# Kernel optimization log

Measured on AMD Instinct MI355X. Metric: run time of the kernel, lower is better.

The kernel has to match this reference:

```python
import jax, jax.numpy as jnp
import numpy as np

N_NODES = 128
F = 64            # hidden channels (64x0e + 64x1o)
N_RBF = 8
H_R = 64          # radial MLP hidden
L = 2             # num_interactions
R_MAX = 5.0
AVG_NEIGH = 127.0
G_DIM = 16
N_SPECIES = 5

# static fully-connected edge list (no self edges): E = n*(n-1)
_idx = np.arange(N_NODES)
_s, _r = np.meshgrid(_idx, _idx, indexing='ij')
_mask = _s != _r
SENDERS = jnp.asarray(_s[_mask])    # [E]
RECEIVERS = jnp.asarray(_r[_mask])  # [E]


def setup_inputs() -> dict:
    key = jax.random.key(0)
    ks = jax.random.split(key, 12)
    inp = {
        'positions': jax.random.normal(ks[0], (32, N_NODES, 3), jnp.float32),
        'node_features': jax.random.randint(ks[1], (32, N_NODES), 0, N_SPECIES),
        'global_features': jax.random.normal(ks[2], (32, G_DIM), jnp.float32),
        # learned parameters
        'embed': jax.random.normal(ks[3], (N_SPECIES, F), jnp.float32) * 0.1,
        'glob_w': jax.random.normal(ks[4], (G_DIM, F), jnp.float32) * 0.1,
        'rbf_w1': jax.random.normal(ks[5], (L, N_RBF, H_R), jnp.float32) * 0.3,
        'rbf_b1': jnp.zeros((L, H_R), jnp.float32),
        'rbf_w2': jax.random.normal(ks[6], (L, H_R, 3 * F), jnp.float32) * 0.1,
        'ws': jax.random.normal(ks[7], (L, F, F), jnp.float32) * 0.1,
        'wv': jax.random.normal(ks[8], (L, F, F), jnp.float32) * 0.1,
        'wout': jax.random.normal(ks[9], (F,), jnp.float32) * 0.1,
        'final_scaling': jnp.ones((), jnp.float32),
    }
    return inp


def _rbf(d):
    # gaussian radial basis on [0, r_max]
    centers = jnp.linspace(0.0, R_MAX, N_RBF)
    width = R_MAX / N_RBF
    return jnp.exp(-((d[:, None] - centers) ** 2) / (2.0 * width * width))  # [E, N_RBF]


def _single(pos, species, glob, embed, glob_w, rbf_w1, rbf_b1, rbf_w2, ws, wv, wout, final_scaling):
    # graph construction + edge vectors
    edge_vec = pos[RECEIVERS] - pos[SENDERS]                 # [E,3]
    d = jnp.sqrt(jnp.sum(edge_vec ** 2, axis=-1) + 1e-12)   # [E]
    unit = edge_vec / d[:, None]                             # [E,3]
    phi = _rbf(d)                                            # [E,N_RBF]

    # node embedding (species one-hot lookup) conditioned on global features
    s = embed[species] + glob @ glob_w                       # [n,F] scalars
    v = jnp.zeros((N_NODES, F, 3), pos.dtype)                # [n,F,3] vectors

    for l in range(L):
        rw = jax.nn.silu(phi @ rbf_w1[l] + rbf_b1[l]) @ rbf_w2[l]  # [E,3F]
        r1, r2, r3 = jnp.split(rw, 3, axis=-1)               # each [E,F]
        ms = r1 * s[SENDERS]                                 # [E,F]
        mv = r2[..., None] * v[SENDERS] + (r3 * s[SENDERS])[..., None] * unit[:, None, :]  # [E,F,3]
        agg_s = jax.ops.segment_sum(ms, RECEIVERS, num_segments=N_NODES) / AVG_NEIGH
        agg_v = jax.ops.segment_sum(mv, RECEIVERS, num_segments=N_NODES) / AVG_NEIGH
        s = s + agg_s @ ws[l]
        v = v + jnp.einsum('nfd,fg->ngd', agg_v, wv[l])

    out = jnp.einsum('nfd,f->nd', v, wout)                   # equivariant readout [n,3]
    return (out - pos) * final_scaling


def reference(positions, node_features, global_features, embed, glob_w, rbf_w1,
              rbf_b1, rbf_w2, ws, wv, wout, final_scaling):
    fn = lambda p, sp, g: _single(p, sp, g, embed, glob_w, rbf_w1, rbf_b1,
                                  rbf_w2, ws, wv, wout, final_scaling)
    return jax.vmap(fn)(positions, node_features, global_features)
```

## Files before the change

kernel.cpp:

```cpp
#include <hip/hip_runtime.h>
#include <hip/hip_bf16.h>


#define NN 128
#define BB 32
#define FF 64

using f32x4  = __attribute__((ext_vector_type(4))) float;
using short8 = __attribute__((ext_vector_type(8))) short;
using half4  = __attribute__((ext_vector_type(4))) _Float16;

__device__ __forceinline__ unsigned short f2bf(float x) {
    unsigned int u = __float_as_uint(x);
    u += 0x7fff + ((u >> 16) & 1);
    return (unsigned short)(u >> 16);
}
__device__ __forceinline__ unsigned int f2bf_fast32(float x) {
    return (__float_as_uint(x) + 0x8000u) >> 16;
}

__global__ __launch_bounds__(256) void setup_kernel(
    const float* __restrict__ w2,
    const float* __restrict__ ws,
    const float* __restrict__ wv,
    const float* __restrict__ rbf_w1,
    const float* __restrict__ rbf_b1,
    const int* __restrict__ species, const float* __restrict__ glob,
    const float* __restrict__ embed, const float* __restrict__ glob_w,
    short* __restrict__ w2frag,
    float* __restrict__ wT4,
    _Float16* __restrict__ w1A,
    float* __restrict__ s)
{
    const int blk = blockIdx.x;
    if (blk < 192) {
        const int tid = blk * 256 + threadIdx.x;
        const int NFRAG = 24576;
        if (tid < NFRAG) {
            const int e  = tid & 7;
            const int l  = (tid >> 3) & 63;
            const int ks = (tid >> 9) & 1;
            const int q  = tid >> 10;
            const int nt = q % 3;
            const int wv_ = (q / 3) & 3;
            const int layer = q / 12;
            const int col = nt * 64 + wv_ * 16 + (l & 15);
            const int hb  = ks * 32 + (l >> 4) * 8 + e;
            const float val = w2[layer * 64 * 192 + hb * 192 + col] * (1.0f / 127.0f);
            w2frag[tid] = (short)f2bf(val);
        }
        const int tid2 = tid - NFRAG;
        if (tid2 >= 0 && tid2 < 16384) {
            const int c   = tid2 & 3;
            const int g   = (tid2 >> 2) & 63;
            const int ff4 = (tid2 >> 8) & 15;
            const int m   = (tid2 >> 12) & 1;
            const int layer = tid2 >> 13;
            const float* src = (m == 0 ? ws : wv) + layer * 4096;
            wT4[tid2] = src[(ff4 * 4 + c) * 64 + g];
        }
        const int tid3 = tid - NFRAG - 16384;
        if (tid3 >= 0 && tid3 < 2048) {
            const int e  = tid3 & 3;
            const int l  = (tid3 >> 2) & 63;
            const int wv_ = (tid3 >> 8) & 3;
            const int layer = tid3 >> 10;
            const int k = (l >> 4) * 4 + e;
            const int h = wv_ * 16 + (l & 15);
            float val = 0.0f;
            if (k < 8)       val = rbf_w1[layer * 512 + k * 64 + h];
            else if (k == 8) val = rbf_b1[layer * 64 + h];
            w1A[tid3] = (_Float16)val;
        }
    } else {
        const int node = (blk - 192) * 4 + (threadIdx.x >> 6);
        const int b = node >> 7;
        const int f = threadIdx.x & 63;
        const int sp = species[node];
        float acc = embed[sp * FF + f];
#pragma unroll
        for (int k = 0; k < 16; ++k)
            acc = fmaf(glob[b * 16 + k], glob_w[k * FF + f], acc);
        s[node * FF + f] = acc;
    }
}

template<int LAYER>
__global__ __launch_bounds__(256, 2) void msg_kernel(
    const float* __restrict__ pos,
    const float* __restrict__ s_in,
    const float* __restrict__ v_in,
    const half4* __restrict__ w1Abuf,
    const short* __restrict__ w2frag,
    const float* __restrict__ wT4,
    const float* __restrict__ wout,
    const float* __restrict__ scale,
    float* __restrict__ s_out,
    float* __restrict__ v_out,
    float* __restrict__ out)
{
    __shared__ unsigned short hid_lds[NN * 64];
    __shared__ float4 unit_lds[NN];
    __shared__ __align__(16) char phi_pool[NN * 32];
    float4 (*agg4)[16] = (float4(*)[16])phi_pool;

    const int blk = blockIdx.x;
    const int xcd = blk & 7;
    const int idx = blk >> 3;
    const int b = xcd * 4 + (idx >> 7);
    const int i = idx & 127;

    const int t = threadIdx.x;
    const int w = t >> 6;
    const int l = t & 63;
    const int node = b * NN + i;
    const float* pb = pos + b * NN * 3;

    short8 bfrag[3][2];
    {
        const short8* wf = (const short8*)w2frag;
#pragma unroll
        for (int nt = 0; nt < 3; ++nt) {
            if (LAYER == 0 && nt == 1) continue;
#pragma unroll
            for (int ks = 0; ks < 2; ++ks)
                bfrag[nt][ks] = wf[((w * 3 + nt) * 2 + ks) * 64 + l];
        }
    }

    {
        const int j = t & 127;
        const int half = t >> 7;
        const float dx = pb[i * 3 + 0] - pb[j * 3 + 0];
        const float dy = pb[i * 3 + 1] - pb[j * 3 + 1];
        const float dz = pb[i * 3 + 2] - pb[j * 3 + 2];
        const float d2 = fmaf(dx, dx, fmaf(dy, dy, fmaf(dz, dz, 1e-12f)));
        const float inv = __builtin_amdgcn_rsqf(d2);
        const float dd = d2 * inv;
        if (half == 0)
            unit_lds[j] = make_float4(dx * inv, dy * inv, dz * inv, 0.0f);
        const _Float16 zf = (_Float16)0.f;
        half4 ph;
#pragma unroll
        for (int r = 0; r < 4; ++r) {
            const float td = dd - (float)(half * 4 + r) * (5.0f / 7.0f);
            ph[r] = (_Float16)__expf(td * td * -1.28f);
        }
        if (j == i) ph = (half4){zf, zf, zf, zf};
        char* rowp = phi_pool + j * 32;
        const int swz = ((j >> 2) & 3) << 3;
        *(half4*)(rowp + ((half * 8) ^ swz)) = ph;
        if (half == 0) {
            half4 bias = {(j == i) ? zf : (_Float16)1.0f, zf, zf, zf};
            *(half4*)(rowp + (16 ^ swz)) = bias;
        } else {
            *(half4*)(rowp + (24 ^ swz)) = (half4){zf, zf, zf, zf};
        }
    }
    __syncthreads();

    {
        const half4 w1a = w1Abuf[w * 64 + l];
        const int jcol = l & 15;
        const int chunk = (l >> 4) * 8;
        const int hbyte = w * 32 + (l >> 4) * 8;
#pragma unroll
        for (int mt = 0; mt < 8; ++mt) {
            const int j = mt * 16 + jcol;
            const half4 bphi = *(const half4*)(
                phi_pool + j * 32 + (chunk ^ (((j >> 2) & 3) << 3)));
            f32x4 pre = __builtin_amdgcn_mfma_f32_16x16x16f16(
                w1a, bphi, (f32x4){0.f, 0.f, 0.f, 0.f}, 0, 0, 0);
            unsigned int pk[2];
#pragma unroll
            for (int p = 0; p < 2; ++p) {
                float sv[2];
#pragma unroll
                for (int q = 0; q < 2; ++q) {
                    const float z = pre[p * 2 + q];
                    const float ex = __expf(-z);
                    sv[q] = z * __builtin_amdgcn_rcpf(1.0f + ex);
                }
                pk[p] = f2bf_fast32(sv[0]) | (f2bf_fast32(sv[1]) << 16);
            }
            const int byte = j * 128 + (hbyte ^ ((j & 7) << 4));
            *(uint2*)((char*)hid_lds + byte) = make_uint2(pk[0], pk[1]);
        }
    }
    __syncthreads();

    const int f    = w * 16 + (l & 15);
    const int jsub = (l >> 4) * 4;
    const float* sb = s_in + b * NN * FF;
    const float4* vb4 = (LAYER > 0) ? ((const float4*)v_in) + b * NN * FF : nullptr;

    float accs = 0.f, av0 = 0.f, av1 = 0.f, av2 = 0.f;

    float sP[4]; float4 vP[4];
#pragma unroll
    for (int reg = 0; reg < 4; ++reg) {
        const int j = jsub + reg;
        sP[reg] = sb[j * FF + f];
        if (LAYER > 0) vP[reg] = vb4[j * FF + f];
    }

#pragma unroll
    for (int mt = 0; mt < 8; ++mt) {
        const int jA = mt * 16 + (l & 15);
        const int base = jA * 128;
        const int sw = (jA & 7) << 4;
        const short8 a0 = *(const short8*)((const char*)hid_lds + base + (((l >> 4) * 16 +  0) ^ sw));
        const short8 a1 = *(const short8*)((const char*)hid_lds + base + (((l >> 4) * 16 + 64) ^ sw));

        f32x4 c0 = (f32x4){0.f, 0.f, 0.f, 0.f};
        f32x4 c1 = (f32x4){0.f, 0.f, 0.f, 0.f};
        f32x4 c2 = (f32x4){0.f, 0.f, 0.f, 0.f};
        c0 = __builtin_amdgcn_mfma_f32_16x16x32_bf16(a0, bfrag[0][0], c0, 0, 0, 0);
        c0 = __builtin_amdgcn_mfma_f32_16x16x32_bf16(a1, bfrag[0][1], c0, 0, 0, 0);
        if (LAYER > 0) {
            c1 = __builtin_amdgcn_mfma_f32_16x16x32_bf16(a0, bfrag[1][0], c1, 0, 0, 0);
            c1 = __builtin_amdgcn_mfma_f32_16x16x32_bf16(a1, bfrag[1][1], c1, 0, 0, 0);
        }
        c2 = __builtin_amdgcn_mfma_f32_16x16x32_bf16(a0, bfrag[2][0], c2, 0, 0, 0);
        c2 = __builtin_amdgcn_mfma_f32_16x16x32_bf16(a1, bfrag[2][1], c2, 0, 0, 0);

        float sN[4]; float4 vN[4];
        if (mt < 7) {
#pragma unroll
            for (int reg = 0; reg < 4; ++reg) {
                const int j = (mt + 1) * 16 + jsub + reg;
                sN[reg] = sb[j * FF + f];
                if (LAYER > 0) vN[reg] = vb4[j * FF + f];
            }
        }

#pragma unroll
        for (int reg = 0; reg < 4; ++reg) {
            const int j  = mt * 16 + jsub + reg;
            const float r1 = c0[reg];
            const float r2 = c1[reg];
            const float r3 = c2[reg];
            const float sj = sP[reg];
            const float r3s = r3 * sj;
            const float4 u = unit_lds[j];
            accs = fmaf(r1, sj, accs);
            av0 = fmaf(r3s, u.x, av0);
            av1 = fmaf(r3s, u.y, av1);
            av2 = fmaf(r3s, u.z, av2);
            if (LAYER > 0) {
                av0 = fmaf(r2, vP[reg].x, av0);
                av1 = fmaf(r2, vP[reg].y, av1);
                av2 = fmaf(r2, vP[reg].z, av2);
            }
        }
#pragma unroll
        for (int reg = 0; reg < 4; ++reg) {
            sP[reg] = sN[reg];
            if (LAYER > 0) vP[reg] = vN[reg];
        }
    }

    accs += __shfl_xor(accs, 16, 64); accs += __shfl_xor(accs, 32, 64);
    av0  += __shfl_xor(av0, 16, 64);  av0  += __shfl_xor(av0, 32, 64);
    av1  += __shfl_xor(av1, 16, 64);  av1  += __shfl_xor(av1, 32, 64);
    av2  += __shfl_xor(av2, 16, 64);  av2  += __shfl_xor(av2, 32, 64);
    if (l < 16) {
        ((float*)agg4)[0 * 64 + f] = accs;
        ((float*)agg4)[1 * 64 + f] = av0;
        ((float*)agg4)[2 * 64 + f] = av1;
        ((float*)agg4)[3 * 64 + f] = av2;
    }
    __syncthreads();

    const int g = l;
    const float4* wv4 = (const float4*)wT4;
    if (LAYER == 0) {
        const int m = (w == 0) ? 0 : 1;
        const int row = (w == 0) ? 0 : w;
        float a = (w == 0) ? s_in[node * FF + g] : 0.0f;
#pragma unroll
        for (int k = 0; k < 16; ++k) {
            const float4 w4 = wv4[(m * 16 + k) * 64 + g];
            const float4 a4 = agg4[row][k];
            a = fmaf(a4.x, w4.x, a); a = fmaf(a4.y, w4.y, a);
            a = fmaf(a4.z, w4.z, a); a = fmaf(a4.w, w4.w, a);
        }
        if (w == 0) s_out[node * FF + g] = a;
        else        v_out[(node * FF + g) * 4 + (w - 1)] = a;
    } else {
        if (w > 0) {
            const int d = w - 1;
            float a = v_in[(node * FF + g) * 4 + d];
#pragma unroll
            for (int k = 0; k < 16; ++k) {
                const float4 w4 = wv4[(16 + k) * 64 + g];
                const float4 a4 = agg4[w][k];
                a = fmaf(a4.x, w4.x, a); a = fmaf(a4.y, w4.y, a);
                a = fmaf(a4.z, w4.z, a); a = fmaf(a4.w, w4.w, a);
            }
            float p = a * wout[g];
#pragma unroll
            for (int off = 1; off < 64; off <<= 1)
                p += __shfl_xor(p, off, 64);
            if (l == 0)
                out[node * 3 + d] = (p - pos[node * 3 + d]) * scale[0];
        }
    }
}

extern "C" void kernel_launch(void* const* d_in, const int* in_sizes, int n_in,
                              void* d_out, int out_size, void* d_ws, size_t ws_size,
                              hipStream_t stream) {
    const float* pos     = (const float*)d_in[0];
    const int*   species = (const int*)  d_in[1];
    const float* glob    = (const float*)d_in[2];
    const float* embed   = (const float*)d_in[3];
    const float* glob_w  = (const float*)d_in[4];
    const float* rbf_w1  = (const float*)d_in[5];
    const float* rbf_b1  = (const float*)d_in[6];
    const float* rbf_w2  = (const float*)d_in[7];
    const float* ws      = (const float*)d_in[8];
    const float* wv      = (const float*)d_in[9];
    const float* wout    = (const float*)d_in[10];
    const float* scale   = (const float*)d_in[11];

    float* wsf = (float*)d_ws;
    float* s0     = wsf;
    float* s1     = wsf + 262144;
    float* v1     = wsf + 524288;
    short* w2frag = (short*)(wsf + 1572864);
    float* wT4    = wsf + 1585152;
    _Float16* w1A = (_Float16*)(wsf + 1601536);
    float* outp = (float*)d_out;

    setup_kernel<<<dim3(192 + BB * NN / 4), 256, 0, stream>>>(
        rbf_w2, ws, wv, rbf_w1, rbf_b1, species, glob, embed, glob_w,
        w2frag, wT4, w1A, s0);

    msg_kernel<0><<<dim3(NN * BB), 256, 0, stream>>>(
        pos, s0, nullptr,
        (const half4*)w1A, w2frag, wT4, wout, scale,
        s1, v1, nullptr);

    msg_kernel<1><<<dim3(NN * BB), 256, 0, stream>>>(
        pos, s1, v1,
        (const half4*)(w1A + 1024), w2frag + 12288, wT4 + 8192, wout, scale,
        nullptr, nullptr, outp);
}
```

Before: 78.95 us.

## Process two receiver nodes per 512-thread block in message kernel

Each message block now handles two receiver nodes using 512 threads (8 waves), with LDS buffers doubled and indexed per node. Grid size is halved. The aim is to amortize per-block fixed costs such as weight-fragment loads and syncs, and to improve occupancy via launch bounds of 512 threads with 4 blocks. The trade-offs are higher LDS use per block and a tighter register budget under the new launch bounds, which may cause spills.

After: 83.56 us. 5.8% more time.

```diff
diff --git a/kernel.cpp b/kernel.cpp
--- a/kernel.cpp
+++ b/kernel.cpp
@@ -86,7 +86,7 @@
 }
 
 template<int LAYER>
-__global__ __launch_bounds__(256, 2) void msg_kernel(
+__global__ __launch_bounds__(512, 4) void msg_kernel(
     const float* __restrict__ pos,
     const float* __restrict__ s_in,
     const float* __restrict__ v_in,
@@ -99,21 +99,23 @@
     float* __restrict__ v_out,
     float* __restrict__ out)
 {
-    __shared__ unsigned short hid_lds[NN * 64];
-    __shared__ float4 unit_lds[NN];
-    __shared__ __align__(16) char phi_pool[NN * 32];
-    float4 (*agg4)[16] = (float4(*)[16])phi_pool;
+    __shared__ unsigned short hid_lds[2 * NN * 64];
+    __shared__ float4 unit_lds[2 * NN];
+    __shared__ __align__(16) char phi_pool[2 * NN * 32];
+    float* aggf = (float*)phi_pool;
 
     const int blk = blockIdx.x;
     const int xcd = blk & 7;
     const int idx = blk >> 3;
-    const int b = xcd * 4 + (idx >> 7);
-    const int i = idx & 127;
+    const int b = xcd * 4 + (idx >> 6);
+    const int ipair = idx & 63;
 
     const int t = threadIdx.x;
     const int w = t >> 6;
     const int l = t & 63;
-    const int node = b * NN + i;
+    const int r = w >> 2;
+    const int ws = w & 3;
+    const int i = ipair * 2 + r;
     const float* pb = pos + b * NN * 3;
 
     short8 bfrag[3][2];
@@ -124,34 +126,36 @@
             if (LAYER == 0 && nt == 1) continue;
 #pragma unroll
             for (int ks = 0; ks < 2; ++ks)
-                bfrag[nt][ks] = wf[((w * 3 + nt) * 2 + ks) * 64 + l];
+                bfrag[nt][ks] = wf[((ws * 3 + nt) * 2 + ks) * 64 + l];
         }
     }
 
     {
         const int j = t & 127;
-        const int half = t >> 7;
-        const float dx = pb[i * 3 + 0] - pb[j * 3 + 0];
-        const float dy = pb[i * 3 + 1] - pb[j * 3 + 1];
-        const float dz = pb[i * 3 + 2] - pb[j * 3 + 2];
+        const int rr = (t >> 7) & 1;
+        const int half = t >> 8;
+        const int ie = ipair * 2 + rr;
+        const float dx = pb[ie * 3 + 0] - pb[j * 3 + 0];
+        const float dy = pb[ie * 3 + 1] - pb[j * 3 + 1];
+        const float dz = pb[ie * 3 + 2] - pb[j * 3 + 2];
         const float d2 = fmaf(dx, dx, fmaf(dy, dy, fmaf(dz, dz, 1e-12f)));
         const float inv = __builtin_amdgcn_rsqf(d2);
         const float dd = d2 * inv;
         if (half == 0)
-            unit_lds[j] = make_float4(dx * inv, dy * inv, dz * inv, 0.0f);
+            unit_lds[rr * NN + j] = make_float4(dx * inv, dy * inv, dz * inv, 0.0f);
         const _Float16 zf = (_Float16)0.f;
         half4 ph;
 #pragma unroll
-        for (int r = 0; r < 4; ++r) {
-            const float td = dd - (float)(half * 4 + r) * (5.0f / 7.0f);
-            ph[r] = (_Float16)__expf(td * td * -1.28f);
-        }
-        if (j == i) ph = (half4){zf, zf, zf, zf};
-        char* rowp = phi_pool + j * 32;
+        for (int rbf = 0; rbf < 4; ++rbf) {
+            const float td = dd - (float)(half * 4 + rbf) * (5.0f / 7.0f);
+            ph[rbf] = (_Float16)__expf(td * td * -1.28f);
+        }
+        if (j == ie) ph = (half4){zf, zf, zf, zf};
+        char* rowp = phi_pool + rr * 4096 + j * 32;
         const int swz = ((j >> 2) & 3) << 3;
         *(half4*)(rowp + ((half * 8) ^ swz)) = ph;
         if (half == 0) {
-            half4 bias = {(j == i) ? zf : (_Float16)1.0f, zf, zf, zf};
+            half4 bias = {(j == ie) ? zf : (_Float16)1.0f, zf, zf, zf};
             *(half4*)(rowp + (16 ^ swz)) = bias;
         } else {
             *(half4*)(rowp + (24 ^ swz)) = (half4){zf, zf, zf, zf};
@@ -160,15 +164,17 @@
     __syncthreads();
 
     {
-        const half4 w1a = w1Abuf[w * 64 + l];
+        const half4 w1a = w1Abuf[ws * 64 + l];
         const int jcol = l & 15;
         const int chunk = (l >> 4) * 8;
-        const int hbyte = w * 32 + (l >> 4) * 8;
+        const int hbyte = ws * 32 + (l >> 4) * 8;
+        const char* phir = phi_pool + r * 4096;
+        char* hidr = (char*)hid_lds + r * 16384;
 #pragma unroll
         for (int mt = 0; mt < 8; ++mt) {
             const int j = mt * 16 + jcol;
             const half4 bphi = *(const half4*)(
-                phi_pool + j * 32 + (chunk ^ (((j >> 2) & 3) << 3)));
+                phir + j * 32 + (chunk ^ (((j >> 2) & 3) << 3)));
             f32x4 pre = __builtin_amdgcn_mfma_f32_16x16x16f16(
                 w1a, bphi, (f32x4){0.f, 0.f, 0.f, 0.f}, 0, 0, 0);
             unsigned int pk[2];
@@ -184,15 +190,17 @@
                 pk[p] = f2bf_fast32(sv[0]) | (f2bf_fast32(sv[1]) << 16);
             }
             const int byte = j * 128 + (hbyte ^ ((j & 7) << 4));
-            *(uint2*)((char*)hid_lds + byte) = make_uint2(pk[0], pk[1]);
+            *(uint2*)(hidr + byte) = make_uint2(pk[0], pk[1]);
         }
     }
     __syncthreads();
 
-    const int f    = w * 16 + (l & 15);
+    const int f    = ws * 16 + (l & 15);
     const int jsub = (l >> 4) * 4;
     const float* sb = s_in + b * NN * FF;
     const float4* vb4 = (LAYER > 0) ? ((const float4*)v_in) + b * NN * FF : nullptr;
+    const char* hidr = (const char*)hid_lds + r * 16384;
+    const float4* unitr = unit_lds + r * NN;
 
     float accs = 0.f, av0 = 0.f, av1 = 0.f, av2 = 0.f;
 
@@ -209,8 +217,8 @@
         const int jA = mt * 16 + (l & 15);
         const int base = jA * 128;
         const int sw = (jA & 7) << 4;
-        const short8 a0 = *(const short8*)((const char*)hid_lds + base + (((l >> 4) * 16 +  0) ^ sw));
-        const short8 a1 = *(const short8*)((const char*)hid_lds + base + (((l >> 4) * 16 + 64) ^ sw));
+        const short8 a0 = *(const short8*)(hidr + base + (((l >> 4) * 16 +  0) ^ sw));
+        const short8 a1 = *(const short8*)(hidr + base + (((l >> 4) * 16 + 64) ^ sw));
 
         f32x4 c0 = (f32x4){0.f, 0.f, 0.f, 0.f};
         f32x4 c1 = (f32x4){0.f, 0.f, 0.f, 0.f};
@@ -242,7 +250,7 @@
             const float r3 = c2[reg];
             const float sj = sP[reg];
             const float r3s = r3 * sj;
-            const float4 u = unit_lds[j];
+            const float4 u = unitr[j];
             accs = fmaf(r1, sj, accs);
             av0 = fmaf(r3s, u.x, av0);
             av1 = fmaf(r3s, u.y, av1);
@@ -265,36 +273,38 @@
     av1  += __shfl_xor(av1, 16, 64);  av1  += __shfl_xor(av1, 32, 64);
     av2  += __shfl_xor(av2, 16, 64);  av2  += __shfl_xor(av2, 32, 64);
     if (l < 16) {
-        ((float*)agg4)[0 * 64 + f] = accs;
-        ((float*)agg4)[1 * 64 + f] = av0;
-        ((float*)agg4)[2 * 64 + f] = av1;
-        ((float*)agg4)[3 * 64 + f] = av2;
+        aggf[r * 256 + 0 * 64 + f] = accs;
+        aggf[r * 256 + 1 * 64 + f] = av0;
+        aggf[r * 256 + 2 * 64 + f] = av1;
+        aggf[r * 256 + 3 * 64 + f] = av2;
     }
     __syncthreads();
 
     const int g = l;
+    const int node = b * NN + i;
     const float4* wv4 = (const float4*)wT4;
+    const float4* agg4 = ((const float4*)phi_pool) + r * 64;
     if (LAYER == 0) {
-        const int m = (w == 0) ? 0 : 1;
-        const int row = (w == 0) ? 0 : w;
-        float a = (w == 0) ? s_in[node * FF + g] : 0.0f;
+        const int m = (ws == 0) ? 0 : 1;
+        const int row = ws;
+        float a = (ws == 0) ? s_in[node * FF + g] : 0.0f;
 #pragma unroll
         for (int k = 0; k < 16; ++k) {
             const float4 w4 = wv4[(m * 16 + k) * 64 + g];
-            const float4 a4 = agg4[row][k];
+            const float4 a4 = agg4[row * 16 + k];
             a = fmaf(a4.x, w4.x, a); a = fmaf(a4.y, w4.y, a);
             a = fmaf(a4.z, w4.z, a); a = fmaf(a4.w, w4.w, a);
         }
-        if (w == 0) s_out[node * FF + g] = a;
-        else        v_out[(node * FF + g) * 4 + (w - 1)] = a;
+        if (ws == 0) s_out[node * FF + g] = a;
+        else         v_out[(node * FF + g) * 4 + (ws - 1)] = a;
     } else {
-        if (w > 0) {
-            const int d = w - 1;
+        if (ws > 0) {
+            const int d = ws - 1;
             float a = v_in[(node * FF + g) * 4 + d];
 #pragma unroll
             for (int k = 0; k < 16; ++k) {
                 const float4 w4 = wv4[(16 + k) * 64 + g];
-                const float4 a4 = agg4[w][k];
+                const float4 a4 = agg4[ws * 16 + k];
                 a = fmaf(a4.x, w4.x, a); a = fmaf(a4.y, w4.y, a);
                 a = fmaf(a4.z, w4.z, a); a = fmaf(a4.w, w4.w, a);
             }
@@ -337,12 +347,12 @@
         rbf_w2, ws, wv, rbf_w1, rbf_b1, species, glob, embed, glob_w,
         w2frag, wT4, w1A, s0);
 
-    msg_kernel<0><<<dim3(NN * BB), 256, 0, stream>>>(
+    msg_kernel<0><<<dim3(NN * BB / 2), 512, 0, stream>>>(
         pos, s0, nullptr,
         (const half4*)w1A, w2frag, wT4, wout, scale,
         s1, v1, nullptr);
 
-    msg_kernel<1><<<dim3(NN * BB), 256, 0, stream>>>(
+    msg_kernel<1><<<dim3(NN * BB / 2), 512, 0, stream>>>(
         pos, s1, v1,
         (const half4*)(w1A + 1024), w2frag + 12288, wT4 + 8192, wout, scale,
         nullptr, nullptr, outp);
```

## Process four receiver nodes per block with double-buffered LDS pipeline

Applied to the files above, without the earlier changes.

Each block now handles four receiver nodes instead of one, cutting the grid by a factor of four and amortizing the per-block loads of weight fragments. LDS buffers for phi, the hidden activations and unit vectors are doubled so the edge setup and radial MLP of the next node can run alongside the message MFMAs and the tail of the current node. This removes per-block launch and setup overhead and separates dependent phases, at the cost of more LDS per block, which may lower occupancy, and fewer blocks to spread across CUs.

Result: slower. 109.1 us (+38.2%).

```diff
diff --git a/kernel.cpp b/kernel.cpp
--- a/kernel.cpp
+++ b/kernel.cpp
@@ -99,22 +99,26 @@
     float* __restrict__ v_out,
     float* __restrict__ out)
 {
-    __shared__ unsigned short hid_lds[NN * 64];
-    __shared__ float4 unit_lds[NN];
-    __shared__ __align__(16) char phi_pool[NN * 32];
-    float4 (*agg4)[16] = (float4(*)[16])phi_pool;
+    __shared__ unsigned short hid_lds[2][NN * 64];
+    __shared__ float4 unit_lds[2][NN];
+    __shared__ __align__(16) char phi_pool[2][NN * 32];
+    __shared__ float4 agg4[4][16];
 
     const int blk = blockIdx.x;
     const int xcd = blk & 7;
     const int idx = blk >> 3;
-    const int b = xcd * 4 + (idx >> 7);
-    const int i = idx & 127;
+    const int b = xcd * 4 + (idx >> 5);
+    const int i0 = (idx & 31) * 4;
 
     const int t = threadIdx.x;
     const int w = t >> 6;
     const int l = t & 63;
-    const int node = b * NN + i;
     const float* pb = pos + b * NN * 3;
+
+    const int f    = w * 16 + (l & 15);
+    const int jsub = (l >> 4) * 4;
+    const float* sb = s_in + b * NN * FF;
+    const float4* vb4 = (LAYER > 0) ? ((const float4*)v_in) + b * NN * FF : nullptr;
 
     short8 bfrag[3][2];
     {
@@ -127,48 +131,49 @@
                 bfrag[nt][ks] = wf[((w * 3 + nt) * 2 + ks) * 64 + l];
         }
     }
-
-    {
+    const half4 w1a = w1Abuf[w * 64 + l];
+
+    auto A1 = [&](int ie, int bf) {
         const int j = t & 127;
         const int half = t >> 7;
-        const float dx = pb[i * 3 + 0] - pb[j * 3 + 0];
-        const float dy = pb[i * 3 + 1] - pb[j * 3 + 1];
-        const float dz = pb[i * 3 + 2] - pb[j * 3 + 2];
+        const float dx = pb[ie * 3 + 0] - pb[j * 3 + 0];
+        const float dy = pb[ie * 3 + 1] - pb[j * 3 + 1];
+        const float dz = pb[ie * 3 + 2] - pb[j * 3 + 2];
         const float d2 = fmaf(dx, dx, fmaf(dy, dy, fmaf(dz, dz, 1e-12f)));
         const float inv = __builtin_amdgcn_rsqf(d2);
         const float dd = d2 * inv;
         if (half == 0)
-            unit_lds[j] = make_float4(dx * inv, dy * inv, dz * inv, 0.0f);
+            unit_lds[bf][j] = make_float4(dx * inv, dy * inv, dz * inv, 0.0f);
         const _Float16 zf = (_Float16)0.f;
         half4 ph;
 #pragma unroll
-        for (int r = 0; r < 4; ++r) {
-            const float td = dd - (float)(half * 4 + r) * (5.0f / 7.0f);
-            ph[r] = (_Float16)__expf(td * td * -1.28f);
-        }
-        if (j == i) ph = (half4){zf, zf, zf, zf};
-        char* rowp = phi_pool + j * 32;
+        for (int rr = 0; rr < 4; ++rr) {
+            const float td = dd - (float)(half * 4 + rr) * (5.0f / 7.0f);
+            ph[rr] = (_Float16)__expf(td * td * -1.28f);
+        }
+        if (j == ie) ph = (half4){zf, zf, zf, zf};
+        char* rowp = phi_pool[bf] + j * 32;
         const int swz = ((j >> 2) & 3) << 3;
         *(half4*)(rowp + ((half * 8) ^ swz)) = ph;
         if (half == 0) {
-            half4 bias = {(j == i) ? zf : (_Float16)1.0f, zf, zf, zf};
+            half4 bias = {(j == ie) ? zf : (_Float16)1.0f, zf, zf, zf};
             *(half4*)(rowp + (16 ^ swz)) = bias;
         } else {
             *(half4*)(rowp + (24 ^ swz)) = (half4){zf, zf, zf, zf};
         }
-    }
-    __syncthreads();
-
-    {
-        const half4 w1a = w1Abuf[w * 64 + l];
+    };
+
+    auto A2 = [&](int bf) {
         const int jcol = l & 15;
         const int chunk = (l >> 4) * 8;
         const int hbyte = w * 32 + (l >> 4) * 8;
+        const char* phir = phi_pool[bf];
+        char* hidr = (char*)hid_lds[bf];
 #pragma unroll
         for (int mt = 0; mt < 8; ++mt) {
             const int j = mt * 16 + jcol;
             const half4 bphi = *(const half4*)(
-                phi_pool + j * 32 + (chunk ^ (((j >> 2) & 3) << 3)));
+                phir + j * 32 + (chunk ^ (((j >> 2) & 3) << 3)));
             f32x4 pre = __builtin_amdgcn_mfma_f32_16x16x16f16(
                 w1a, bphi, (f32x4){0.f, 0.f, 0.f, 0.f}, 0, 0, 0);
             unsigned int pk[2];
@@ -184,127 +189,138 @@
                 pk[p] = f2bf_fast32(sv[0]) | (f2bf_fast32(sv[1]) << 16);
             }
             const int byte = j * 128 + (hbyte ^ ((j & 7) << 4));
-            *(uint2*)((char*)hid_lds + byte) = make_uint2(pk[0], pk[1]);
-        }
-    }
-    __syncthreads();
-
-    const int f    = w * 16 + (l & 15);
-    const int jsub = (l >> 4) * 4;
-    const float* sb = s_in + b * NN * FF;
-    const float4* vb4 = (LAYER > 0) ? ((const float4*)v_in) + b * NN * FF : nullptr;
-
-    float accs = 0.f, av0 = 0.f, av1 = 0.f, av2 = 0.f;
-
-    float sP[4]; float4 vP[4];
-#pragma unroll
-    for (int reg = 0; reg < 4; ++reg) {
-        const int j = jsub + reg;
-        sP[reg] = sb[j * FF + f];
-        if (LAYER > 0) vP[reg] = vb4[j * FF + f];
-    }
-
-#pragma unroll
-    for (int mt = 0; mt < 8; ++mt) {
-        const int jA = mt * 16 + (l & 15);
-        const int base = jA * 128;
-        const int sw = (jA & 7) << 4;
-        const short8 a0 = *(const short8*)((const char*)hid_lds + base + (((l >> 4) * 16 +  0) ^ sw));
-        const short8 a1 = *(const short8*)((const char*)hid_lds + base + (((l >> 4) * 16 + 64) ^ sw));
-
-        f32x4 c0 = (f32x4){0.f, 0.f, 0.f, 0.f};
-        f32x4 c1 = (f32x4){0.f, 0.f, 0.f, 0.f};
-        f32x4 c2 = (f32x4){0.f, 0.f, 0.f, 0.f};
-        c0 = __builtin_amdgcn_mfma_f32_16x16x32_bf16(a0, bfrag[0][0], c0, 0, 0, 0);
-        c0 = __builtin_amdgcn_mfma_f32_16x16x32_bf16(a1, bfrag[0][1], c0, 0, 0, 0);
-        if (LAYER > 0) {
-            c1 = __builtin_amdgcn_mfma_f32_16x16x32_bf16(a0, bfrag[1][0], c1, 0, 0, 0);
-            c1 = __builtin_amdgcn_mfma_f32_16x16x32_bf16(a1, bfrag[1][1], c1, 0, 0, 0);
-        }
-        c2 = __builtin_amdgcn_mfma_f32_16x16x32_bf16(a0, bfrag[2][0], c2, 0, 0, 0);
-        c2 = __builtin_amdgcn_mfma_f32_16x16x32_bf16(a1, bfrag[2][1], c2, 0, 0, 0);
-
-        float sN[4]; float4 vN[4];
-        if (mt < 7) {
+            *(uint2*)(hidr + byte) = make_uint2(pk[0], pk[1]);
+        }
+    };
+
+    auto BC = [&](int bf) {
+        const char* hidr = (const char*)hid_lds[bf];
+        const float4* unitr = unit_lds[bf];
+        float accs = 0.f, av0 = 0.f, av1 = 0.f, av2 = 0.f;
+        float sP[4]; float4 vP[4];
+#pragma unroll
+        for (int reg = 0; reg < 4; ++reg) {
+            const int j = jsub + reg;
+            sP[reg] = sb[j * FF + f];
+            if (LAYER > 0) vP[reg] = vb4[j * FF + f];
+        }
+#pragma unroll
+        for (int mt = 0; mt < 8; ++mt) {
+            const int jA = mt * 16 + (l & 15);
+            const int base = jA * 128;
+            const int sw = (jA & 7) << 4;
+            const short8 a0 = *(const short8*)(hidr + base + (((l >> 4) * 16 +  0) ^ sw));
+            const short8 a1 = *(const short8*)(hidr + base + (((l >> 4) * 16 + 64) ^ sw));
+
+            f32x4 c0 = (f32x4){0.f, 0.f, 0.f, 0.f};
+            f32x4 c1 = (f32x4){0.f, 0.f, 0.f, 0.f};
+            f32x4 c2 = (f32x4){0.f, 0.f, 0.f, 0.f};
+            c0 = __builtin_amdgcn_mfma_f32_16x16x32_bf16(a0, bfrag[0][0], c0, 0, 0, 0);
+            c0 = __builtin_amdgcn_mfma_f32_16x16x32_bf16(a1, bfrag[0][1], c0, 0, 0, 0);
+            if (LAYER > 0) {
+                c1 = __builtin_amdgcn_mfma_f32_16x16x32_bf16(a0, bfrag[1][0], c1, 0, 0, 0);
+                c1 = __builtin_amdgcn_mfma_f32_16x16x32_bf16(a1, bfrag[1][1], c1, 0, 0, 0);
+            }
+            c2 = __builtin_amdgcn_mfma_f32_16x16x32_bf16(a0, bfrag[2][0], c2, 0, 0, 0);
+            c2 = __builtin_amdgcn_mfma_f32_16x16x32_bf16(a1, bfrag[2][1], c2, 0, 0, 0);
+
+            float sN[4]; float4 vN[4];
+            if (mt < 7) {
+#pragma unroll
+                for (int reg = 0; reg < 4; ++reg) {
+                    const int j = (mt + 1) * 16 + jsub + reg;
+                    sN[reg] = sb[j * FF + f];
+                    if (LAYER > 0) vN[reg] = vb4[j * FF + f];
+                }
+            }
 #pragma unroll
             for (int reg = 0; reg < 4; ++reg) {
-                const int j = (mt + 1) * 16 + jsub + reg;
-                sN[reg] = sb[j * FF + f];
-                if (LAYER > 0) vN[reg] = vb4[j * FF + f];
-            }
-        }
-
-#pragma unroll
-        for (int reg = 0; reg < 4; ++reg) {
-            const int j  = mt * 16 + jsub + reg;
-            const float r1 = c0[reg];
-            const float r2 = c1[reg];
-            const float r3 = c2[reg];
-            const float sj = sP[reg];
-            const float r3s = r3 * sj;
-            const float4 u = unit_lds[j];
-            accs = fmaf(r1, sj, accs);
-            av0 = fmaf(r3s, u.x, av0);
-            av1 = fmaf(r3s, u.y, av1);
-            av2 = fmaf(r3s, u.z, av2);
-            if (LAYER > 0) {
-                av0 = fmaf(r2, vP[reg].x, av0);
-                av1 = fmaf(r2, vP[reg].y, av1);
-                av2 = fmaf(r2, vP[reg].z, av2);
-            }
-        }
-#pragma unroll
-        for (int reg = 0; reg < 4; ++reg) {
-            sP[reg] = sN[reg];
-            if (LAYER > 0) vP[reg] = vN[reg];
-        }
-    }
-
-    accs += __shfl_xor(accs, 16, 64); accs += __shfl_xor(accs, 32, 64);
-    av0  += __shfl_xor(av0, 16, 64);  av0  += __shfl_xor(av0, 32, 64);
-    av1  += __shfl_xor(av1, 16, 64);  av1  += __shfl_xor(av1, 32, 64);
-    av2  += __shfl_xor(av2, 16, 64);  av2  += __shfl_xor(av2, 32, 64);
-    if (l < 16) {
-        ((float*)agg4)[0 * 64 + f] = accs;
-        ((float*)agg4)[1 * 64 + f] = av0;
-        ((float*)agg4)[2 * 64 + f] = av1;
-        ((float*)agg4)[3 * 64 + f] = av2;
-    }
-    __syncthreads();
-
-    const int g = l;
-    const float4* wv4 = (const float4*)wT4;
-    if (LAYER == 0) {
-        const int m = (w == 0) ? 0 : 1;
-        const int row = (w == 0) ? 0 : w;
-        float a = (w == 0) ? s_in[node * FF + g] : 0.0f;
-#pragma unroll
-        for (int k = 0; k < 16; ++k) {
-            const float4 w4 = wv4[(m * 16 + k) * 64 + g];
-            const float4 a4 = agg4[row][k];
-            a = fmaf(a4.x, w4.x, a); a = fmaf(a4.y, w4.y, a);
-            a = fmaf(a4.z, w4.z, a); a = fmaf(a4.w, w4.w, a);
-        }
-        if (w == 0) s_out[node * FF + g] = a;
-        else        v_out[(node * FF + g) * 4 + (w - 1)] = a;
-    } else {
-        if (w > 0) {
-            const int d = w - 1;
-            float a = v_in[(node * FF + g) * 4 + d];
+                const int j  = mt * 16 + jsub + reg;
+                const float r1 = c0[reg];
+                const float r2 = c1[reg];
+                const float r3 = c2[reg];
+                const float sj = sP[reg];
+                const float r3s = r3 * sj;
+                const float4 u = unitr[j];
+                accs = fmaf(r1, sj, accs);
+                av0 = fmaf(r3s, u.x, av0);
+                av1 = fmaf(r3s, u.y, av1);
+                av2 = fmaf(r3s, u.z, av2);
+                if (LAYER > 0) {
+                    av0 = fmaf(r2, vP[reg].x, av0);
+                    av1 = fmaf(r2, vP[reg].y, av1);
+                    av2 = fmaf(r2, vP[reg].z, av2);
+                }
+            }
+#pragma unroll
+            for (int reg = 0; reg < 4; ++reg) {
+                sP[reg] = sN[reg];
+                if (LAYER > 0) vP[reg] = vN[reg];
+            }
+        }
+        accs += __shfl_xor(accs, 16, 64); accs += __shfl_xor(accs, 32, 64);
+        av0  += __shfl_xor(av0, 16, 64);  av0  += __shfl_xor(av0, 32, 64);
+        av1  += __shfl_xor(av1, 16, 64);  av1  += __shfl_xor(av1, 32, 64);
+        av2  += __shfl_xor(av2, 16, 64);  av2  += __shfl_xor(av2, 32, 64);
+        if (l < 16) {
+            ((float*)agg4)[0 * 64 + f] = accs;
+            ((float*)agg4)[1 * 64 + f] = av0;
+            ((float*)agg4)[2 * 64 + f] = av1;
+            ((float*)agg4)[3 * 64 + f] = av2;
+        }
+    };
+
+    auto TAIL = [&](int ie) {
+        const int g = l;
+        const int node = b * NN + ie;
+        const float4* wv4 = (const float4*)wT4;
+        if (LAYER == 0) {
+            const int m = (w == 0) ? 0 : 1;
+            const int row = (w == 0) ? 0 : w;
+            float a = (w == 0) ? s_in[node * FF + g] : 0.0f;
 #pragma unroll
             for (int k = 0; k < 16; ++k) {
-                const float4 w4 = wv4[(16 + k) * 64 + g];
-                const float4 a4 = agg4[w][k];
+                const float4 w4 = wv4[(m * 16 + k) * 64 + g];
+                const float4 a4 = agg4[row][k];
                 a = fmaf(a4.x, w4.x, a); a = fmaf(a4.y, w4.y, a);
                 a = fmaf(a4.z, w4.z, a); a = fmaf(a4.w, w4.w, a);
             }
-            float p = a * wout[g];
-#pragma unroll
-            for (int off = 1; off < 64; off <<= 1)
-                p += __shfl_xor(p, off, 64);
-            if (l == 0)
-                out[node * 3 + d] = (p - pos[node * 3 + d]) * scale[0];
-        }
+            if (w == 0) s_out[node * FF + g] = a;
+            else        v_out[(node * FF + g) * 4 + (w - 1)] = a;
+        } else {
+            if (w > 0) {
+                const int d = w - 1;
+                float a = v_in[(node * FF + g) * 4 + d];
+#pragma unroll
+                for (int k = 0; k < 16; ++k) {
+                    const float4 w4 = wv4[(16 + k) * 64 + g];
+                    const float4 a4 = agg4[w][k];
+                    a = fmaf(a4.x, w4.x, a); a = fmaf(a4.y, w4.y, a);
+                    a = fmaf(a4.z, w4.z, a); a = fmaf(a4.w, w4.w, a);
+                }
+                float p = a * wout[g];
+#pragma unroll
+                for (int off = 1; off < 64; off <<= 1)
+                    p += __shfl_xor(p, off, 64);
+                if (l == 0)
+                    out[node * 3 + d] = (p - pos[node * 3 + d]) * scale[0];
+            }
+        }
+    };
+
+    A1(i0, 0);
+    __syncthreads();
+    A2(0);
+    __syncthreads();
+#pragma unroll
+    for (int it = 0; it < 4; ++it) {
+        const int cur = it & 1;
+        if (it < 3) A1(i0 + it + 1, cur ^ 1);
+        BC(cur);
+        __syncthreads();
+        if (it < 3) A2(cur ^ 1);
+        TAIL(i0 + it);
+        __syncthreads();
     }
 }
 
@@ -337,12 +353,12 @@
         rbf_w2, ws, wv, rbf_w1, rbf_b1, species, glob, embed, glob_w,
         w2frag, wT4, w1A, s0);
 
-    msg_kernel<0><<<dim3(NN * BB), 256, 0, stream>>>(
+    msg_kernel<0><<<dim3(NN * BB / 4), 256, 0, stream>>>(
         pos, s0, nullptr,
         (const half4*)w1A, w2frag, wT4, wout, scale,
         s1, v1, nullptr);
 
-    msg_kernel<1><<<dim3(NN * BB), 256, 0, stream>>>(
+    msg_kernel<1><<<dim3(NN * BB / 4), 256, 0, stream>>>(
         pos, s1, v1,
         (const half4*)(w1A + 1024), w2frag + 12288, wT4 + 8192, wout, scale,
         nullptr, nullptr, outp);
```
